# Kernel optimization log

Hardware: AMD Instinct MI355X
Metric: run time of the kernel (lower is better)

The kernel has to match this reference:

```python
import math
import jax, jax.numpy as jnp
import numpy as np

VOCAB, EMB, ADIM, HEADS = 32000, 512, 64, 8
B, S = 8, 1024
SIGMOID_DOMAIN = 5.0
LN_EPS = 1e-5


def setup_inputs() -> dict:
    key = jax.random.key(0)
    k = jax.random.split(key, 7)
    x = jax.random.randint(k[0], (B, S), 0, VOCAB, dtype=jnp.int64 if jax.config.read('jax_enable_x64') else jnp.int32)
    emb_table = jax.random.normal(k[1], (VOCAB, EMB), dtype=jnp.float32)
    gamma = jnp.ones((EMB,), dtype=jnp.float32)
    beta = jnp.zeros((EMB,), dtype=jnp.float32)
    # torch.rand -> uniform [0, 1)
    Wq = jax.random.uniform(k[2], (HEADS, ADIM, EMB), dtype=jnp.float32)
    Wk = jax.random.uniform(k[3], (HEADS, ADIM, EMB), dtype=jnp.float32)
    Wv = jax.random.uniform(k[4], (HEADS, EMB, EMB), dtype=jnp.float32)
    return {"x": x, "emb_table": emb_table, "gamma": gamma, "beta": beta,
            "Wq": Wq, "Wk": Wk, "Wv": Wv}


def reference(x, emb_table, gamma, beta, Wq, Wk, Wv):
    # Embedding + LayerNorm -> [B, S, E]
    e = emb_table[x]
    mu = jnp.mean(e, axis=-1, keepdims=True)
    var = jnp.mean((e - mu) ** 2, axis=-1, keepdims=True)
    h = (e - mu) / jnp.sqrt(var + LN_EPS) * gamma + beta

    # per-head projections: W [H, A, E] x h [B, S, E] -> [B, H, S, A]
    q = jnp.einsum('hae,bse->bhsa', Wq, h)
    k = jnp.einsum('hae,bse->bhsa', Wk, h)
    v = jnp.einsum('hve,bse->bhsv', Wv, h)  # v_dim == E

    scale = math.sqrt(EMB)
    scores = jnp.einsum('bhsa,bhta->bhst', q, k) / scale  # [B, H, S, S]

    # overtaking-sigmoid: per-row min-max normalize, blend softmax with sigmoid
    s_max = jnp.max(scores, axis=-1, keepdims=True)
    s_min = jnp.min(scores, axis=-1, keepdims=True)
    sn = (scores - s_min) / (s_max - s_min)
    softmax_sel = 1.0 - jnp.max(sn, axis=-1, keepdims=True)
    sigmoid_sel = 1.0 - softmax_sel
    weights = (softmax_sel * jax.nn.softmax(sn, axis=-1)
               + sigmoid_sel * jax.nn.sigmoid(sn * (2.0 * SIGMOID_DOMAIN) - SIGMOID_DOMAIN))

    out = jnp.einsum('bhst,bhtv->bhsv', weights, v)  # [B, H, S, E]
    return out
```

## Files before the change

### kernel.cpp

```cpp
#include <hip/hip_runtime.h>
#include <math.h>

#define NB 8
#define NH 8
#define NS 1024
#define NE 512
#define NA 64
#define NBH (NB*NH)

typedef short s8v __attribute__((ext_vector_type(8)));
typedef float f4v __attribute__((ext_vector_type(4)));
typedef unsigned short u4v __attribute__((ext_vector_type(4)));

#define MFMA16(a,b,c) __builtin_amdgcn_mfma_f32_16x16x32_bf16((a),(b),(c),0,0,0)

static __device__ __forceinline__ unsigned short f2bf(float f) {
    union { float f; unsigned u; } c; c.f = f;
    unsigned r = c.u + 0x7FFF + ((c.u >> 16) & 1);
    return (unsigned short)(r >> 16);
}
static __device__ __forceinline__ s8v ld8(const unsigned short* p) {
    return *(const s8v*)p;
}
static __device__ __forceinline__ void gload16(const unsigned short* g, unsigned short* l) {
    __builtin_amdgcn_global_load_lds(
        (const __attribute__((address_space(1))) unsigned char*)g,
        (__attribute__((address_space(3))) unsigned char*)l, 16, 0, 0);
}

static __device__ __forceinline__ void stage_tile(
    const unsigned short* src, size_t stride, int k0,
    unsigned short* lds, int tid)
{
    int w = tid >> 6, l = tid & 63;
    #pragma unroll
    for (int c = 0; c < 4; ++c) {
        int chunk = w * 4 + c;
        int row = chunk * 8 + (l >> 3);
        gload16(src + (size_t)row * stride + k0 + (l & 7) * 8,
                lds + chunk * 512 + l * 8);
    }
}

__global__ __launch_bounds__(256) void k_embed_ln(
    const int* __restrict__ x, const float* __restrict__ emb,
    const float* __restrict__ gamma, const float* __restrict__ beta,
    unsigned short* __restrict__ hb)
{
    int row = blockIdx.x;
    int tok = x[row];
    const float* e = emb + (size_t)tok * NE;
    int t = threadIdx.x;
    float v0 = e[t], v1 = e[t + 256];
    float sum = v0 + v1, ssq = v0 * v0 + v1 * v1;
    #pragma unroll
    for (int o = 32; o > 0; o >>= 1) {
        sum += __shfl_xor(sum, o);
        ssq += __shfl_xor(ssq, o);
    }
    __shared__ float wsum[4], wssq[4];
    __shared__ float mu_s, rstd_s;
    int wid = t >> 6;
    if ((t & 63) == 0) { wsum[wid] = sum; wssq[wid] = ssq; }
    __syncthreads();
    if (t == 0) {
        float S1 = wsum[0] + wsum[1] + wsum[2] + wsum[3];
        float S2 = wssq[0] + wssq[1] + wssq[2] + wssq[3];
        float mu = S1 / NE;
        float var = S2 / NE - mu * mu;
        mu_s = mu;
        rstd_s = rsqrtf(var + 1e-5f);
    }
    __syncthreads();
    float mu = mu_s, rstd = rstd_s;
    unsigned short* hr = hb + (size_t)row * NE;
    hr[t]       = f2bf((v0 - mu) * rstd * gamma[t]       + beta[t]);
    hr[t + 256] = f2bf((v1 - mu) * rstd * gamma[t + 256] + beta[t + 256]);
}

__global__ __launch_bounds__(256) void k_cvt3(
    const float* __restrict__ Wq, const float* __restrict__ Wk,
    const float* __restrict__ Wv,
    unsigned short* __restrict__ wqb, unsigned short* __restrict__ wkb,
    unsigned short* __restrict__ wvb, int nqk, int nv)
{
    int i = blockIdx.x * 256 + threadIdx.x;
    if (i < nqk)            wqb[i] = f2bf(Wq[i]);
    else if (i < 2 * nqk)   wkb[i - nqk] = f2bf(Wk[i - nqk]);
    else if (i < 2 * nqk + nv) wvb[i - 2 * nqk] = f2bf(Wv[i - 2 * nqk]);
}

__global__ __launch_bounds__(256) void k_qk_gemm(
    const unsigned short* __restrict__ hb, const unsigned short* __restrict__ wqb,
    const unsigned short* __restrict__ wkb,
    unsigned short* __restrict__ qb, unsigned short* __restrict__ kbf)
{
    int bid = blockIdx.x;
    int b2 = (bid & 7) * 64 + (bid >> 3);
    int st = b2 & 7, bh = b2 >> 3;
    int b = bh >> 3, hh = bh & 7;
    int tid = threadIdx.x;
    int w = tid >> 6, l = tid & 63;
    int lo = l & 15, hi = l >> 4;
    int wr = w >> 1, wc = w & 1;

    __shared__ __align__(16) unsigned short As[128 * 64];
    __shared__ __align__(16) unsigned short Bs[128 * 64];

    f4v acc[4][4];
    f4v z = {0.f, 0.f, 0.f, 0.f};
    #pragma unroll
    for (int i = 0; i < 4; ++i)
        #pragma unroll
        for (int j = 0; j < 4; ++j) acc[i][j] = z;

    const unsigned short* asrc = hb + ((size_t)(b * NS) + st * 128) * NE;
    for (int kt = 0; kt < 8; ++kt) {
        int k0 = kt * 64;
        stage_tile(asrc, NE, k0, As, tid);
        {
            #pragma unroll
            for (int c = 0; c < 4; ++c) {
                int chunk = w * 4 + c;
                int row = chunk * 8 + (l >> 3);
                const unsigned short* bsrc = (chunk < 8)
                    ? wqb + ((size_t)(hh * NA) + row) * NE
                    : wkb + ((size_t)(hh * NA) + row - 64) * NE;
                gload16(bsrc + k0 + (l & 7) * 8, Bs + chunk * 512 + l * 8);
            }
        }
        __syncthreads();
        #pragma unroll
        for (int ks = 0; ks < 2; ++ks) {
            s8v af[4], bf[4];
            #pragma unroll
            for (int sub = 0; sub < 4; ++sub)
                af[sub] = ld8(As + (wr * 64 + sub * 16 + lo) * 64 + ks * 32 + hi * 8);
            #pragma unroll
            for (int es = 0; es < 4; ++es)
                bf[es] = ld8(Bs + (wc * 64 + es * 16 + lo) * 64 + ks * 32 + hi * 8);
            #pragma unroll
            for (int sub = 0; sub < 4; ++sub)
                #pragma unroll
                for (int es = 0; es < 4; ++es)
                    acc[sub][es] = MFMA16(af[sub], bf[es], acc[sub][es]);
        }
        __syncthreads();
    }
    unsigned short* dst = (wc == 0) ? qb : kbf;
    #pragma unroll
    for (int sub = 0; sub < 4; ++sub)
        #pragma unroll
        for (int es = 0; es < 4; ++es)
            #pragma unroll
            for (int i = 0; i < 4; ++i) {
                int s = st * 128 + wr * 64 + sub * 16 + hi * 4 + i;
                int a = es * 16 + lo;
                dst[((size_t)bh * NS + s) * NA + a] = f2bf(acc[sub][es][i]);
            }
}

__global__ __launch_bounds__(256) void k_v_gemm(
    const unsigned short* __restrict__ hb, const unsigned short* __restrict__ wvb,
    unsigned short* __restrict__ vtb)
{
    int bid = blockIdx.x;
    int b2 = (bid & 7) * 256 + (bid >> 3);
    int tt = b2 & 7;
    int et = (b2 >> 3) & 3;
    int bh = b2 >> 5;
    int b = bh >> 3, hh = bh & 7;
    int tid = threadIdx.x;
    int w = tid >> 6, l = tid & 63;
    int lo = l & 15, hi = l >> 4;
    int wr = w >> 1, wc = w & 1;

    __shared__ __align__(16) unsigned short As[128 * 64];
    __shared__ __align__(16) unsigned short Bs[128 * 64];

    f4v acc[4][4];
    f4v z = {0.f, 0.f, 0.f, 0.f};
    #pragma unroll
    for (int i = 0; i < 4; ++i)
        #pragma unroll
        for (int j = 0; j < 4; ++j) acc[i][j] = z;

    const unsigned short* asrc = wvb + ((size_t)(hh * NE) + et * 128) * NE;
    const unsigned short* bsrc = hb + ((size_t)(b * NS) + tt * 128) * NE;
    for (int kt = 0; kt < 8; ++kt) {
        int k0 = kt * 64;
        stage_tile(asrc, NE, k0, As, tid);
        stage_tile(bsrc, NE, k0, Bs, tid);
        __syncthreads();
        #pragma unroll
        for (int ks = 0; ks < 2; ++ks) {
            s8v af[4], bf[4];
            #pragma unroll
            for (int sub = 0; sub < 4; ++sub)
                af[sub] = ld8(As + (wr * 64 + sub * 16 + lo) * 64 + ks * 32 + hi * 8);
            #pragma unroll
            for (int es = 0; es < 4; ++es)
                bf[es] = ld8(Bs + (wc * 64 + es * 16 + lo) * 64 + ks * 32 + hi * 8);
            #pragma unroll
            for (int sub = 0; sub < 4; ++sub)
                #pragma unroll
                for (int es = 0; es < 4; ++es)
                    acc[sub][es] = MFMA16(af[sub], bf[es], acc[sub][es]);
        }
        __syncthreads();
    }
    #pragma unroll
    for (int sub = 0; sub < 4; ++sub)
        #pragma unroll
        for (int es = 0; es < 4; ++es)
            #pragma unroll
            for (int i = 0; i < 4; ++i) {
                int e_ = et * 128 + wr * 64 + sub * 16 + hi * 4 + i;
                int t_ = tt * 128 + wc * 64 + es * 16 + lo;
                vtb[((size_t)bh * NE + e_) * NS + t_] = f2bf(acc[sub][es][i]);
            }
}

#define WSTR 136
__global__ __launch_bounds__(512, 2) void k_attn_fused(
    const unsigned short* __restrict__ qb, const unsigned short* __restrict__ kbf,
    const unsigned short* __restrict__ vtb, float* __restrict__ out)
{
    int bid = blockIdx.x;
    int b2 = (bid & 7) * 64 + (bid >> 3);
    int qt = b2 & 7, bh = b2 >> 3;
    int s0 = qt * 128;
    int tid = threadIdx.x;
    int w = tid >> 6, l = tid & 63;
    int lo = l & 15, hi = l >> 4;

    __shared__ __align__(16) unsigned short Qs[128 * 64];
    __shared__ __align__(16) unsigned short wt[2][128 * WSTR];
    __shared__ float pmn[8][128], pmx[8][128];

    #pragma unroll
    for (int j = 0; j < 2; ++j) {
        int ch = j * 512 + tid;
        int row = ch >> 3, cc = ch & 7;
        s8v qv = ld8(qb + ((size_t)bh * NS + s0 + row) * NA + cc * 8);
        *(s8v*)(Qs + row * 64 + ((cc ^ (row & 7)) * 8)) = qv;
    }

    const unsigned short* kframe = kbf + (size_t)bh * NS * NA;
    const unsigned short* vbase = vtb + ((size_t)bh * NE + w * 64) * NS;

    auto loadK = [&](int t0, s8v& k0, s8v& k1) {
        const unsigned short* kp = kframe + (size_t)(t0 + w * 16 + lo) * NA + hi * 8;
        k0 = ld8(kp);
        k1 = ld8(kp + 32);
    };
    auto loadQ = [&](int sub, s8v& q0, s8v& q1) {
        int r = sub * 16 + lo;
        q0 = ld8(Qs + r * 64 + ((hi ^ (lo & 7)) * 8));
        q1 = ld8(Qs + r * 64 + (((hi + 4) ^ (lo & 7)) * 8));
    };

    f4v z = {0.f, 0.f, 0.f, 0.f};
    s8v kc0, kc1, kn0, kn1;

    __syncthreads();
    float mnp[8], mxp[8];
    #pragma unroll
    for (int sub = 0; sub < 8; ++sub) { mnp[sub] = 1e30f; mxp[sub] = -1e30f; }
    loadK(0, kc0, kc1);
    for (int it = 0; it < 8; ++it) {
        if (it < 7) loadK((it + 1) * 128, kn0, kn1);
        #pragma unroll
        for (int sub = 0; sub < 8; ++sub) {
            s8v q0, q1;
            loadQ(sub, q0, q1);
            f4v c = z;
            c = MFMA16(kc0, q0, c);
            c = MFMA16(kc1, q1, c);
            mnp[sub] = fminf(mnp[sub], fminf(fminf(c[0], c[1]), fminf(c[2], c[3])));
            mxp[sub] = fmaxf(mxp[sub], fmaxf(fmaxf(c[0], c[1]), fmaxf(c[2], c[3])));
        }
        kc0 = kn0; kc1 = kn1;
    }
    #pragma unroll
    for (int sub = 0; sub < 8; ++sub) {
        mnp[sub] = fminf(mnp[sub], __shfl_xor(mnp[sub], 16));
        mnp[sub] = fminf(mnp[sub], __shfl_xor(mnp[sub], 32));
        mxp[sub] = fmaxf(mxp[sub], __shfl_xor(mxp[sub], 16));
        mxp[sub] = fmaxf(mxp[sub], __shfl_xor(mxp[sub], 32));
    }
    if (l < 16) {
        #pragma unroll
        for (int sub = 0; sub < 8; ++sub) {
            pmn[w][sub * 16 + l] = mnp[sub];
            pmx[w][sub * 16 + l] = mxp[sub];
        }
    }
    __syncthreads();
    float invv[8], n2v[8];
    #pragma unroll
    for (int sub = 0; sub < 8; ++sub) {
        int q = sub * 16 + lo;
        float mn = pmn[0][q], mx = pmx[0][q];
        #pragma unroll
        for (int j = 1; j < 8; ++j) {
            mn = fminf(mn, pmn[j][q]);
            mx = fmaxf(mx, pmx[j][q]);
        }
        float iv = __builtin_amdgcn_rcpf(mx - mn);
        invv[sub] = iv;
        n2v[sub] = -mn * iv;
    }

    f4v acc[8][4];
    #pragma unroll
    for (int sub = 0; sub < 8; ++sub)
        #pragma unroll
        for (int es = 0; es < 4; ++es) acc[sub][es] = z;

    auto scores = [&](s8v k0, s8v k1, unsigned short* wbuf) {
        #pragma unroll
        for (int sub = 0; sub < 8; ++sub) {
            s8v q0, q1;
            loadQ(sub, q0, q1);
            f4v c = z;
            c = MFMA16(k0, q0, c);
            c = MFMA16(k1, q1, c);
            u4v pk;
            #pragma unroll
            for (int i = 0; i < 4; ++i) {
                float sn = fmaf(c[i], invv[sub], n2v[sub]);
                float arg = fmaf(sn, -14.4269504089f, 7.2134752044f);
                float e = __builtin_amdgcn_exp2f(arg);
                pk[i] = f2bf(__builtin_amdgcn_rcpf(1.f + e));
            }
            *(u4v*)(wbuf + (sub * 16 + lo) * WSTR + w * 16 + hi * 4) = pk;
        }
    };

    loadK(0, kc0, kc1);
    scores(kc0, kc1, wt[0]);
    for (int it = 0; it < 8; ++it) {
        int t0 = it * 128;
        if (it < 7) loadK(t0 + 128, kn0, kn1);
        asm volatile("s_waitcnt lgkmcnt(0)" ::: "memory");
        __builtin_amdgcn_s_barrier();
        __builtin_amdgcn_sched_barrier(0);
        {
            const unsigned short* wb = wt[it & 1];
            #pragma unroll
            for (int ks = 0; ks < 4; ++ks) {
                s8v bv[4];
                #pragma unroll
                for (int es = 0; es < 4; ++es)
                    bv[es] = ld8(vbase + (size_t)(es * 16 + lo) * NS + t0 + ks * 32 + hi * 8);
                #pragma unroll
                for (int sub = 0; sub < 8; ++sub) {
                    s8v aw = ld8(wb + (sub * 16 + lo) * WSTR + ks * 32 + hi * 8);
                    #pragma unroll
                    for (int es = 0; es < 4; ++es)
                        acc[sub][es] = MFMA16(aw, bv[es], acc[sub][es]);
                }
            }
        }
        if (it < 7) scores(kn0, kn1, wt[(it + 1) & 1]);
    }
    #pragma unroll
    for (int sub = 0; sub < 8; ++sub)
        #pragma unroll
        for (int es = 0; es < 4; ++es)
            #pragma unroll
            for (int i = 0; i < 4; ++i)
                out[((size_t)bh * NS + s0 + sub * 16 + hi * 4 + i) * NE
                    + w * 64 + es * 16 + lo] = acc[sub][es][i];
}

extern "C" void kernel_launch(void* const* d_in, const int* in_sizes, int n_in,
                              void* d_out, int out_size, void* d_ws, size_t ws_size,
                              hipStream_t stream) {
    const int*   x     = (const int*)d_in[0];
    const float* emb   = (const float*)d_in[1];
    const float* gamma = (const float*)d_in[2];
    const float* beta  = (const float*)d_in[3];
    const float* Wq    = (const float*)d_in[4];
    const float* Wk    = (const float*)d_in[5];
    const float* Wv    = (const float*)d_in[6];
    float* out = (float*)d_out;

    unsigned short* p = (unsigned short*)d_ws;
    unsigned short* hb  = p;  p += (size_t)NB * NS * NE;
    unsigned short* qb  = p;  p += (size_t)NBH * NS * NA;
    unsigned short* kb  = p;  p += (size_t)NBH * NS * NA;
    unsigned short* vtb = p;  p += (size_t)NBH * NS * NE;
    unsigned short* wqb = p;  p += (size_t)NH * NA * NE;
    unsigned short* wkb = p;  p += (size_t)NH * NA * NE;
    unsigned short* wvb = p;  p += (size_t)NH * NE * NE;

    const int nqk = NH * NA * NE, nv = NH * NE * NE;
    k_cvt3<<<(2 * nqk + nv + 255) / 256, 256, 0, stream>>>(Wq, Wk, Wv, wqb, wkb, wvb, nqk, nv);
    k_embed_ln<<<NB * NS, 256, 0, stream>>>(x, emb, gamma, beta, hb);
    k_qk_gemm<<<512, 256, 0, stream>>>(hb, wqb, wkb, qb, kb);
    k_v_gemm<<<2048, 256, 0, stream>>>(hb, wvb, vtb);
    k_attn_fused<<<512, 512, 0, stream>>>(qb, kb, vtb, out);
}
```

Baseline: 214.8 us.

## Merge prep and projection kernels, XOR-swizzle attention weight LDS tile

Merges the weight-conversion and embed+LayerNorm kernels into one launch, and the QK and V projection GEMMs into another, selected by block index. This cuts the launch count from five to three and lets independent work share the GPU. The attention kernel's weight buffer drops its padded stride of 136 for an unpadded 128-wide row with an XOR swizzle on 8-element chunks, which shrinks LDS use while trying to avoid bank conflicts. The risk is that the swizzle mapping may not be conflict-free, and the merged kernels carry branch-divergent resource usage.

```diff
diff --git a/kernel.cpp b/kernel.cpp
--- a/kernel.cpp
+++ b/kernel.cpp
@@ -42,63 +42,59 @@
     }
 }
 
-__global__ __launch_bounds__(256) void k_embed_ln(
+__global__ __launch_bounds__(256) void k_prep(
     const int* __restrict__ x, const float* __restrict__ emb,
     const float* __restrict__ gamma, const float* __restrict__ beta,
-    unsigned short* __restrict__ hb)
-{
-    int row = blockIdx.x;
-    int tok = x[row];
-    const float* e = emb + (size_t)tok * NE;
-    int t = threadIdx.x;
-    float v0 = e[t], v1 = e[t + 256];
-    float sum = v0 + v1, ssq = v0 * v0 + v1 * v1;
-    #pragma unroll
-    for (int o = 32; o > 0; o >>= 1) {
-        sum += __shfl_xor(sum, o);
-        ssq += __shfl_xor(ssq, o);
-    }
-    __shared__ float wsum[4], wssq[4];
-    __shared__ float mu_s, rstd_s;
-    int wid = t >> 6;
-    if ((t & 63) == 0) { wsum[wid] = sum; wssq[wid] = ssq; }
-    __syncthreads();
-    if (t == 0) {
-        float S1 = wsum[0] + wsum[1] + wsum[2] + wsum[3];
-        float S2 = wssq[0] + wssq[1] + wssq[2] + wssq[3];
-        float mu = S1 / NE;
-        float var = S2 / NE - mu * mu;
-        mu_s = mu;
-        rstd_s = rsqrtf(var + 1e-5f);
-    }
-    __syncthreads();
-    float mu = mu_s, rstd = rstd_s;
-    unsigned short* hr = hb + (size_t)row * NE;
-    hr[t]       = f2bf((v0 - mu) * rstd * gamma[t]       + beta[t]);
-    hr[t + 256] = f2bf((v1 - mu) * rstd * gamma[t + 256] + beta[t + 256]);
-}
-
-__global__ __launch_bounds__(256) void k_cvt3(
     const float* __restrict__ Wq, const float* __restrict__ Wk,
     const float* __restrict__ Wv,
+    unsigned short* __restrict__ hb,
     unsigned short* __restrict__ wqb, unsigned short* __restrict__ wkb,
     unsigned short* __restrict__ wvb, int nqk, int nv)
 {
-    int i = blockIdx.x * 256 + threadIdx.x;
-    if (i < nqk)            wqb[i] = f2bf(Wq[i]);
-    else if (i < 2 * nqk)   wkb[i - nqk] = f2bf(Wk[i - nqk]);
-    else if (i < 2 * nqk + nv) wvb[i - 2 * nqk] = f2bf(Wv[i - 2 * nqk]);
-}
-
-__global__ __launch_bounds__(256) void k_qk_gemm(
+    if (blockIdx.x < NB * NS) {
+        int row = blockIdx.x;
+        int tok = x[row];
+        const float* e = emb + (size_t)tok * NE;
+        int t = threadIdx.x;
+        float v0 = e[t], v1 = e[t + 256];
+        float sum = v0 + v1, ssq = v0 * v0 + v1 * v1;
+        #pragma unroll
+        for (int o = 32; o > 0; o >>= 1) {
+            sum += __shfl_xor(sum, o);
+            ssq += __shfl_xor(ssq, o);
+        }
+        __shared__ float wsum[4], wssq[4];
+        __shared__ float mu_s, rstd_s;
+        int wid = t >> 6;
+        if ((t & 63) == 0) { wsum[wid] = sum; wssq[wid] = ssq; }
+        __syncthreads();
+        if (t == 0) {
+            float S1 = wsum[0] + wsum[1] + wsum[2] + wsum[3];
+            float S2 = wssq[0] + wssq[1] + wssq[2] + wssq[3];
+            float mu = S1 / NE;
+            float var = S2 / NE - mu * mu;
+            mu_s = mu;
+            rstd_s = rsqrtf(var + 1e-5f);
+        }
+        __syncthreads();
+        float mu = mu_s, rstd = rstd_s;
+        unsigned short* hr = hb + (size_t)row * NE;
+        hr[t]       = f2bf((v0 - mu) * rstd * gamma[t]       + beta[t]);
+        hr[t + 256] = f2bf((v1 - mu) * rstd * gamma[t + 256] + beta[t + 256]);
+    } else {
+        int i = (blockIdx.x - NB * NS) * 256 + threadIdx.x;
+        if (i < nqk)               wqb[i] = f2bf(Wq[i]);
+        else if (i < 2 * nqk)      wkb[i - nqk] = f2bf(Wk[i - nqk]);
+        else if (i < 2 * nqk + nv) wvb[i - 2 * nqk] = f2bf(Wv[i - 2 * nqk]);
+    }
+}
+
+__global__ __launch_bounds__(256) void k_proj(
     const unsigned short* __restrict__ hb, const unsigned short* __restrict__ wqb,
-    const unsigned short* __restrict__ wkb,
-    unsigned short* __restrict__ qb, unsigned short* __restrict__ kbf)
+    const unsigned short* __restrict__ wkb, const unsigned short* __restrict__ wvb,
+    unsigned short* __restrict__ qb, unsigned short* __restrict__ kbf,
+    unsigned short* __restrict__ vtb)
 {
-    int bid = blockIdx.x;
-    int b2 = (bid & 7) * 64 + (bid >> 3);
-    int st = b2 & 7, bh = b2 >> 3;
-    int b = bh >> 3, hh = bh & 7;
     int tid = threadIdx.x;
     int w = tid >> 6, l = tid & 63;
     int lo = l & 15, hi = l >> 4;
@@ -114,114 +110,101 @@
         #pragma unroll
         for (int j = 0; j < 4; ++j) acc[i][j] = z;
 
-    const unsigned short* asrc = hb + ((size_t)(b * NS) + st * 128) * NE;
-    for (int kt = 0; kt < 8; ++kt) {
-        int k0 = kt * 64;
-        stage_tile(asrc, NE, k0, As, tid);
-        {
-            #pragma unroll
-            for (int c = 0; c < 4; ++c) {
-                int chunk = w * 4 + c;
-                int row = chunk * 8 + (l >> 3);
-                const unsigned short* bsrc = (chunk < 8)
-                    ? wqb + ((size_t)(hh * NA) + row) * NE
-                    : wkb + ((size_t)(hh * NA) + row - 64) * NE;
-                gload16(bsrc + k0 + (l & 7) * 8, Bs + chunk * 512 + l * 8);
-            }
-        }
-        __syncthreads();
-        #pragma unroll
-        for (int ks = 0; ks < 2; ++ks) {
-            s8v af[4], bf[4];
-            #pragma unroll
-            for (int sub = 0; sub < 4; ++sub)
-                af[sub] = ld8(As + (wr * 64 + sub * 16 + lo) * 64 + ks * 32 + hi * 8);
+    if (blockIdx.x < 512) {
+        int bid = blockIdx.x;
+        int b2 = (bid & 7) * 64 + (bid >> 3);
+        int st = b2 & 7, bh = b2 >> 3;
+        int b = bh >> 3, hh = bh & 7;
+
+        const unsigned short* asrc = hb + ((size_t)(b * NS) + st * 128) * NE;
+        for (int kt = 0; kt < 8; ++kt) {
+            int k0 = kt * 64;
+            stage_tile(asrc, NE, k0, As, tid);
+            {
+                #pragma unroll
+                for (int c = 0; c < 4; ++c) {
+                    int chunk = w * 4 + c;
+                    int row = chunk * 8 + (l >> 3);
+                    const unsigned short* bsrc = (chunk < 8)
+                        ? wqb + ((size_t)(hh * NA) + row) * NE
+                        : wkb + ((size_t)(hh * NA) + row - 64) * NE;
+                    gload16(bsrc + k0 + (l & 7) * 8, Bs + chunk * 512 + l * 8);
+                }
+            }
+            __syncthreads();
+            #pragma unroll
+            for (int ks = 0; ks < 2; ++ks) {
+                s8v af[4], bf[4];
+                #pragma unroll
+                for (int sub = 0; sub < 4; ++sub)
+                    af[sub] = ld8(As + (wr * 64 + sub * 16 + lo) * 64 + ks * 32 + hi * 8);
+                #pragma unroll
+                for (int es = 0; es < 4; ++es)
+                    bf[es] = ld8(Bs + (wc * 64 + es * 16 + lo) * 64 + ks * 32 + hi * 8);
+                #pragma unroll
+                for (int sub = 0; sub < 4; ++sub)
+                    #pragma unroll
+                    for (int es = 0; es < 4; ++es)
+                        acc[sub][es] = MFMA16(af[sub], bf[es], acc[sub][es]);
+            }
+            __syncthreads();
+        }
+        unsigned short* dst = (wc == 0) ? qb : kbf;
+        #pragma unroll
+        for (int sub = 0; sub < 4; ++sub)
             #pragma unroll
             for (int es = 0; es < 4; ++es)
-                bf[es] = ld8(Bs + (wc * 64 + es * 16 + lo) * 64 + ks * 32 + hi * 8);
-            #pragma unroll
-            for (int sub = 0; sub < 4; ++sub)
+                #pragma unroll
+                for (int i = 0; i < 4; ++i) {
+                    int s = st * 128 + wr * 64 + sub * 16 + hi * 4 + i;
+                    int a = es * 16 + lo;
+                    dst[((size_t)bh * NS + s) * NA + a] = f2bf(acc[sub][es][i]);
+                }
+    } else {
+        int bid = blockIdx.x - 512;
+        int b2 = (bid & 7) * 256 + (bid >> 3);
+        int tt = b2 & 7;
+        int et = (b2 >> 3) & 3;
+        int bh = b2 >> 5;
+        int b = bh >> 3, hh = bh & 7;
+
+        const unsigned short* asrc = wvb + ((size_t)(hh * NE) + et * 128) * NE;
+        const unsigned short* bsrc = hb + ((size_t)(b * NS) + tt * 128) * NE;
+        for (int kt = 0; kt < 8; ++kt) {
+            int k0 = kt * 64;
+            stage_tile(asrc, NE, k0, As, tid);
+            stage_tile(bsrc, NE, k0, Bs, tid);
+            __syncthreads();
+            #pragma unroll
+            for (int ks = 0; ks < 2; ++ks) {
+                s8v af[4], bf[4];
+                #pragma unroll
+                for (int sub = 0; sub < 4; ++sub)
+                    af[sub] = ld8(As + (wr * 64 + sub * 16 + lo) * 64 + ks * 32 + hi * 8);
                 #pragma unroll
                 for (int es = 0; es < 4; ++es)
-                    acc[sub][es] = MFMA16(af[sub], bf[es], acc[sub][es]);
-        }
-        __syncthreads();
-    }
-    unsigned short* dst = (wc == 0) ? qb : kbf;
-    #pragma unroll
-    for (int sub = 0; sub < 4; ++sub)
-        #pragma unroll
-        for (int es = 0; es < 4; ++es)
-            #pragma unroll
-            for (int i = 0; i < 4; ++i) {
-                int s = st * 128 + wr * 64 + sub * 16 + hi * 4 + i;
-                int a = es * 16 + lo;
-                dst[((size_t)bh * NS + s) * NA + a] = f2bf(acc[sub][es][i]);
-            }
-}
-
-__global__ __launch_bounds__(256) void k_v_gemm(
-    const unsigned short* __restrict__ hb, const unsigned short* __restrict__ wvb,
-    unsigned short* __restrict__ vtb)
-{
-    int bid = blockIdx.x;
-    int b2 = (bid & 7) * 256 + (bid >> 3);
-    int tt = b2 & 7;
-    int et = (b2 >> 3) & 3;
-    int bh = b2 >> 5;
-    int b = bh >> 3, hh = bh & 7;
-    int tid = threadIdx.x;
-    int w = tid >> 6, l = tid & 63;
-    int lo = l & 15, hi = l >> 4;
-    int wr = w >> 1, wc = w & 1;
-
-    __shared__ __align__(16) unsigned short As[128 * 64];
-    __shared__ __align__(16) unsigned short Bs[128 * 64];
-
-    f4v acc[4][4];
-    f4v z = {0.f, 0.f, 0.f, 0.f};
-    #pragma unroll
-    for (int i = 0; i < 4; ++i)
-        #pragma unroll
-        for (int j = 0; j < 4; ++j) acc[i][j] = z;
-
-    const unsigned short* asrc = wvb + ((size_t)(hh * NE) + et * 128) * NE;
-    const unsigned short* bsrc = hb + ((size_t)(b * NS) + tt * 128) * NE;
-    for (int kt = 0; kt < 8; ++kt) {
-        int k0 = kt * 64;
-        stage_tile(asrc, NE, k0, As, tid);
-        stage_tile(bsrc, NE, k0, Bs, tid);
-        __syncthreads();
-        #pragma unroll
-        for (int ks = 0; ks < 2; ++ks) {
-            s8v af[4], bf[4];
-            #pragma unroll
-            for (int sub = 0; sub < 4; ++sub)
-                af[sub] = ld8(As + (wr * 64 + sub * 16 + lo) * 64 + ks * 32 + hi * 8);
+                    bf[es] = ld8(Bs + (wc * 64 + es * 16 + lo) * 64 + ks * 32 + hi * 8);
+                #pragma unroll
+                for (int sub = 0; sub < 4; ++sub)
+                    #pragma unroll
+                    for (int es = 0; es < 4; ++es)
+                        acc[sub][es] = MFMA16(af[sub], bf[es], acc[sub][es]);
+            }
+            __syncthreads();
+        }
+        #pragma unroll
+        for (int sub = 0; sub < 4; ++sub)
             #pragma unroll
             for (int es = 0; es < 4; ++es)
-                bf[es] = ld8(Bs + (wc * 64 + es * 16 + lo) * 64 + ks * 32 + hi * 8);
-            #pragma unroll
-            for (int sub = 0; sub < 4; ++sub)
-                #pragma unroll
-                for (int es = 0; es < 4; ++es)
-                    acc[sub][es] = MFMA16(af[sub], bf[es], acc[sub][es]);
-        }
-        __syncthreads();
-    }
-    #pragma unroll
-    for (int sub = 0; sub < 4; ++sub)
-        #pragma unroll
-        for (int es = 0; es < 4; ++es)
-            #pragma unroll
-            for (int i = 0; i < 4; ++i) {
-                int e_ = et * 128 + wr * 64 + sub * 16 + hi * 4 + i;
-                int t_ = tt * 128 + wc * 64 + es * 16 + lo;
-                vtb[((size_t)bh * NE + e_) * NS + t_] = f2bf(acc[sub][es][i]);
-            }
-}
-
-#define WSTR 136
+                #pragma unroll
+                for (int i = 0; i < 4; ++i) {
+                    int e_ = et * 128 + wr * 64 + sub * 16 + hi * 4 + i;
+                    int t_ = tt * 128 + wc * 64 + es * 16 + lo;
+                    vtb[((size_t)bh * NE + e_) * NS + t_] = f2bf(acc[sub][es][i]);
+                }
+    }
+}
+
 __global__ __launch_bounds__(512, 2) void k_attn_fused(
     const unsigned short* __restrict__ qb, const unsigned short* __restrict__ kbf,
     const unsigned short* __restrict__ vtb, float* __restrict__ out)
@@ -235,7 +218,7 @@
     int lo = l & 15, hi = l >> 4;
 
     __shared__ __align__(16) unsigned short Qs[128 * 64];
-    __shared__ __align__(16) unsigned short wt[2][128 * WSTR];
+    __shared__ __align__(16) unsigned short wt[2][128 * 128];
     __shared__ float pmn[8][128], pmx[8][128];
 
     #pragma unroll
@@ -318,6 +301,8 @@
         #pragma unroll
         for (int es = 0; es < 4; ++es) acc[sub][es] = z;
 
+    int cw = w * 2 + (hi >> 1);
+    int whalf = (hi & 1) * 4;
     auto scores = [&](s8v k0, s8v k1, unsigned short* wbuf) {
         #pragma unroll
         for (int sub = 0; sub < 8; ++sub) {
@@ -334,7 +319,7 @@
                 float e = __builtin_amdgcn_exp2f(arg);
                 pk[i] = f2bf(__builtin_amdgcn_rcpf(1.f + e));
             }
-            *(u4v*)(wbuf + (sub * 16 + lo) * WSTR + w * 16 + hi * 4) = pk;
+            *(u4v*)(wbuf + (sub * 16 + lo) * 128 + ((cw ^ (lo & 7)) * 8) + whalf) = pk;
         }
     };
 
@@ -356,7 +341,7 @@
                     bv[es] = ld8(vbase + (size_t)(es * 16 + lo) * NS + t0 + ks * 32 + hi * 8);
                 #pragma unroll
                 for (int sub = 0; sub < 8; ++sub) {
-                    s8v aw = ld8(wb + (sub * 16 + lo) * WSTR + ks * 32 + hi * 8);
+                    s8v aw = ld8(wb + (sub * 16 + lo) * 128 + (((ks * 4 + hi) ^ (lo & 7)) * 8));
                     #pragma unroll
                     for (int es = 0; es < 4; ++es)
                         acc[sub][es] = MFMA16(aw, bv[es], acc[sub][es]);
@@ -397,9 +382,9 @@
     unsigned short* wvb = p;  p += (size_t)NH * NE * NE;
 
     const int nqk = NH * NA * NE, nv = NH * NE * NE;
-    k_cvt3<<<(2 * nqk + nv + 255) / 256, 256, 0, stream>>>(Wq, Wk, Wv, wqb, wkb, wvb, nqk, nv);
-    k_embed_ln<<<NB * NS, 256, 0, stream>>>(x, emb, gamma, beta, hb);
-    k_qk_gemm<<<512, 256, 0, stream>>>(hb, wqb, wkb, qb, kb);
-    k_v_gemm<<<2048, 256, 0, stream>>>(hb, wvb, vtb);
+    const int cvt_blocks = (2 * nqk + nv + 255) / 256;
+    k_prep<<<NB * NS + cvt_blocks, 256, 0, stream>>>(
+        x, emb, gamma, beta, Wq, Wk, Wv, hb, wqb, wkb, wvb, nqk, nv);
+    k_proj<<<512 + 2048, 256, 0, stream>>>(hb, wqb, wkb, wvb, qb, kb, vtb);
     k_attn_fused<<<512, 512, 0, stream>>>(qb, kb, vtb, out);
 }
```

After: 208.9 us. 1.03x faster.
